# Kernel tuning notes

Measured on AMD Instinct MI355X. Metric: run time of the kernel, lower is better.

## Reference

```python
import jax, jax.numpy as jnp
import numpy as np
import math

B, S, D, H = 2, 2048, 1024, 16
DK = D // H
NUM_BUCKETS = 32
MAX_DISTANCE = 128


def _relative_position_bucket(relative_position, num_buckets=NUM_BUCKETS, max_distance=MAX_DISTANCE):
    # Bidirectional bucketing, faithful to the torch implementation.
    nb = num_buckets // 2
    n = -relative_position
    ret = (n < 0).astype(jnp.int32) * nb
    n = jnp.abs(n)
    max_exact = nb // 2
    is_small = n < max_exact
    # guard log(0); is_small branch covers n < max_exact anyway
    val_if_large = max_exact + (
        jnp.log(jnp.maximum(n, 1).astype(jnp.float32) / max_exact)
        / math.log(max_distance / max_exact)
        * (nb - max_exact)
    ).astype(jnp.int32)
    val_if_large = jnp.minimum(val_if_large, nb - 1)
    return ret + jnp.where(is_small, n, val_if_large)


def setup_inputs() -> dict:
    key = jax.random.key(0)
    ks = jax.random.split(key, 6)
    scale = 1.0 / math.sqrt(D)
    return {
        "hidden_states": jax.random.normal(ks[0], (B, S, D), dtype=jnp.float32),
        "Wq": jax.random.normal(ks[1], (D, D), dtype=jnp.float32) * scale,
        "Wk": jax.random.normal(ks[2], (D, D), dtype=jnp.float32) * scale,
        "Wv": jax.random.normal(ks[3], (D, D), dtype=jnp.float32) * scale,
        "Wo": jax.random.normal(ks[4], (D, D), dtype=jnp.float32) * scale,
        "rel_emb": jax.random.normal(ks[5], (NUM_BUCKETS, H), dtype=jnp.float32) * 0.1,
    }


def reference(hidden_states, Wq, Wk, Wv, Wo, rel_emb):
    b, s, d = hidden_states.shape
    # nn.Linear convention: y = x @ W.T
    q = jnp.einsum("bsd,ed->bse", hidden_states, Wq).reshape(b, s, H, DK).transpose(0, 2, 1, 3)
    k = jnp.einsum("bsd,ed->bse", hidden_states, Wk).reshape(b, s, H, DK).transpose(0, 2, 1, 3)
    v = jnp.einsum("bsd,ed->bse", hidden_states, Wv).reshape(b, s, H, DK).transpose(0, 2, 1, 3)
    scores = jnp.einsum("bhqd,bhkd->bhqk", q, k) / math.sqrt(DK)  # [B,H,S,S]
    # T5 relative position bias
    ctx = jnp.arange(s)[:, None]
    mem = jnp.arange(s)[None, :]
    rp_bucket = _relative_position_bucket(mem - ctx)          # [S,S]
    bias = rel_emb[rp_bucket]                                  # [S,S,H]
    bias = bias.transpose(2, 0, 1)[None]                       # [1,H,S,S]
    scores = scores + bias
    attn = jax.nn.softmax(scores, axis=-1)
    out = jnp.einsum("bhqk,bhkd->bhqd", attn, v)               # [B,H,S,DK]
    out = out.transpose(0, 2, 1, 3).reshape(b, s, d)
    return jnp.einsum("bsd,ed->bse", out, Wo)
```

## Files before the change

### kernel.cpp

```cpp
#include <hip/hip_runtime.h>
#include <hip/hip_bf16.h>
#include <cstdint>
#include <cstddef>

typedef __bf16 bf16;
typedef __attribute__((ext_vector_type(8))) __bf16 bf16x8;
typedef __attribute__((ext_vector_type(4))) __bf16 bf16x4;
typedef __attribute__((ext_vector_type(4))) float f32x4;
typedef __attribute__((ext_vector_type(4))) short s16x4;

#define B_ 2
#define S_ 2048
#define D_ 1024
#define H_ 16
#define DK_ 64
#define NROWS (B_*S_)
#define NBIAS 4095
#define LDQ 3072
#define LOG2E 1.44269504f

__device__ __forceinline__ void async16(void* lds, const void* g) {
  __builtin_amdgcn_global_load_lds(
      (const __attribute__((address_space(1))) void*)g,
      (__attribute__((address_space(3))) void*)lds, 16, 0, 0);
}

__device__ __forceinline__ f32x4 mfma16(bf16x8 a, bf16x8 b, f32x4 c) {
  return __builtin_amdgcn_mfma_f32_16x16x32_bf16(a, b, c, 0, 0, 0);
}

__device__ __forceinline__ s16x4 bc4(bf16x4 x) {
  union { bf16x4 b; s16x4 s; } u; u.b = x; return u.s;
}

__device__ __forceinline__ f32x4 mfma16k(bf16x4 a, bf16x4 b, f32x4 c) {
  return __builtin_amdgcn_mfma_f32_16x16x16bf16_1k(bc4(a), bc4(b), c, 0, 0, 0);
}

__device__ __forceinline__ float exp2_hw(float x) {
  return __builtin_amdgcn_exp2f(x);
}

__global__ void prep_kernel(const float* __restrict__ X,
                            const float* __restrict__ Wq, const float* __restrict__ Wk,
                            const float* __restrict__ Wv, const float* __restrict__ Wo,
                            const float* __restrict__ rel_emb,
                            bf16* __restrict__ Xb, bf16* __restrict__ oqkv,
                            bf16* __restrict__ oo, float* __restrict__ tab) {
  const int bid = blockIdx.x;
  const int tid = threadIdx.x;
  if (bid < 4096) {
    int i = bid * 256 + tid;
    float4 v = ((const float4*)X)[i];
    bf16x4 o;
    o[0] = (bf16)v.x; o[1] = (bf16)v.y; o[2] = (bf16)v.z; o[3] = (bf16)v.w;
    ((bf16x4*)Xb)[i] = o;
  } else if (bid < 8192) {
    int widx = bid - 4096;
    int y = widx >> 10;
    const float* src = (y == 0) ? Wq : (y == 1) ? Wk : (y == 2) ? Wv : Wo;
    bf16* dst = (y < 3) ? (oqkv + (size_t)y * D_ * D_) : oo;
    int i = (widx & 1023) * 256 + tid;
    float4 v = ((const float4*)src)[i];
    bf16x4 o;
    o[0] = (bf16)v.x; o[1] = (bf16)v.y; o[2] = (bf16)v.z; o[3] = (bf16)v.w;
    ((bf16x4*)dst)[i] = o;
  } else {
    int idx = (bid - 8192) * 256 + tid;
    if (idx >= H_ * NBIAS) return;
    int h = idx / NBIAS;
    int p = idx - h * NBIAS;
    int rel = p - 2047;
    int n = -rel;
    int ret = 0;
    if (n < 0) { ret = 16; n = -n; }
    int bucket;
    if (n < 8) {
      bucket = ret + n;
    } else {
      double v = log((double)n / 8.0) / log(16.0) * 8.0;
      int vi = 8 + (int)v;
      if (vi > 15) vi = 15;
      bucket = ret + vi;
    }
    tab[idx] = rel_emb[bucket * H_ + h] * LOG2E;
  }
}

template<int OUT_BF16, int MF, int VT_EP>
__global__ __launch_bounds__(256, 3)
void gemm_bt(const bf16* __restrict__ A, const bf16* __restrict__ Bw,
             void* __restrict__ C, bf16* __restrict__ VT, int vThr,
             int M, int N, int K, int colThr, float a0, float a1) {
  __shared__ bf16 smem[MF * 32 * 64 + 128 * 64];
  bf16* As = smem;
  bf16* Bs = smem + MF * 32 * 64;
  const int tid = threadIdx.x;
  const int lane = tid & 63;
  const int w = tid >> 6;
  const int wr = w >> 1, wc = w & 1;
  const int l15 = lane & 15, lhi = lane >> 4;
  const int m0 = blockIdx.y * (MF * 32), n0 = blockIdx.x * 128;
  const float alpha = (n0 < colThr) ? a0 : a1;

  f32x4 acc[MF][4] = {};

  const int urow = tid >> 3;
  const int uswz = (tid & 7) ^ (urow & 7);
  const bf16* ga = A  + (size_t)(m0 + urow) * K + uswz * 8;
  const bf16* gb = Bw + (size_t)(n0 + urow) * K + uswz * 8;

  for (int kt = 0; kt < K; kt += 64) {
#pragma unroll
    for (int rnd = 0; rnd < MF; ++rnd)
      async16(As + tid * 8 + rnd * 2048, ga + kt + (size_t)(rnd * 32) * K);
#pragma unroll
    for (int rnd = 0; rnd < 4; ++rnd)
      async16(Bs + tid * 8 + rnd * 2048, gb + kt + (size_t)(rnd * 32) * K);
    __syncthreads();

#pragma unroll
    for (int kc = 0; kc < 2; ++kc) {
      bf16x8 af[MF], bfr[4];
#pragma unroll
      for (int m = 0; m < MF; ++m) {
        int row = wr * (MF * 16) + m * 16 + l15;
        int off = (row * 64 + kc * 32 + lhi * 8) ^ ((row & 7) << 3);
        af[m] = *(const bf16x8*)&As[off];
      }
#pragma unroll
      for (int n = 0; n < 4; ++n) {
        int row = wc * 64 + n * 16 + l15;
        int off = (row * 64 + kc * 32 + lhi * 8) ^ ((row & 7) << 3);
        bfr[n] = *(const bf16x8*)&Bs[off];
      }
      __builtin_amdgcn_s_setprio(1);
#pragma unroll
      for (int m = 0; m < MF; ++m)
#pragma unroll
        for (int n = 0; n < 4; ++n)
          acc[m][n] = mfma16(af[m], bfr[n], acc[m][n]);
      __builtin_amdgcn_s_setprio(0);
    }
    __syncthreads();
  }

  if (VT_EP && n0 >= vThr) {
    bf16* T = smem;
#pragma unroll
    for (int m = 0; m < MF; ++m)
#pragma unroll
      for (int n = 0; n < 4; ++n)
#pragma unroll
        for (int r = 0; r < 4; ++r) {
          int rl = wr * (MF * 16) + m * 16 + lhi * 4 + r;
          int cl = wc * 64 + n * 16 + l15;
          T[cl * 128 + (rl ^ ((cl & 7) << 3))] = (bf16)(acc[m][n][r] * alpha);
        }
    __syncthreads();
    const int bb = m0 >> 11, s0l = m0 & 2047, d0 = n0 - vThr;
    const int dr = tid >> 1, sh = tid & 1;
    bf16* dst = VT + ((size_t)(bb * 1024 + d0 + dr)) * 2048 + s0l + sh * 64;
    const bf16* src = T + dr * 128;
#pragma unroll
    for (int i = 0; i < 8; ++i) {
      int sb = sh * 8 + i;
      *(bf16x8*)(dst + i * 8) = *(const bf16x8*)(src + ((sb ^ (dr & 7)) * 8));
    }
    return;
  }

#pragma unroll
  for (int m = 0; m < MF; ++m)
#pragma unroll
    for (int n = 0; n < 4; ++n)
#pragma unroll
      for (int r = 0; r < 4; ++r) {
        int row = m0 + wr * (MF * 16) + m * 16 + lhi * 4 + r;
        int col = n0 + wc * 64 + n * 16 + l15;
        float v = acc[m][n][r] * alpha;
        if (OUT_BF16) ((bf16*)C)[(size_t)row * N + col] = (bf16)v;
        else          ((float*)C)[(size_t)row * N + col] = v;
      }
}

__global__ __launch_bounds__(256, 2)
void attn_fwd(const bf16* __restrict__ QKV, const bf16* __restrict__ VTg_,
              const float* __restrict__ biasTab, const float* __restrict__ rel_emb,
              bf16* __restrict__ Og) {
  __shared__ bf16 Ks[2][64 * 64];
  __shared__ bf16 VTs[2][64 * 64];
  __shared__ float bias_s[512];
  const int tid = threadIdx.x;
  const int lane = tid & 63, w = tid >> 6;
  const int l15 = lane & 15, lhi = lane >> 4;
  const int wg = blockIdx.x;
  const int bh = wg & 31, qt = wg >> 5;
  const int b = bh >> 4, h = bh & 15;
  const int q0 = qt * 128;

  for (int i = tid; i < 511; i += 256)
    bias_s[i] = biasTab[h * NBIAS + 1792 + i];

  const float cL = rel_emb[15 * H_ + h] * LOG2E;
  const float cR = rel_emb[31 * H_ + h] * LOG2E;

  bf16x8 qa[2][2];
  {
    const bf16* Qbase = QKV + (size_t)(b * S_ + q0 + w * 32) * LDQ + h * DK_;
#pragma unroll
    for (int qf = 0; qf < 2; ++qf)
#pragma unroll
      for (int c = 0; c < 2; ++c)
        qa[qf][c] = *(const bf16x8*)(Qbase + (size_t)(qf * 16 + l15) * LDQ + c * 32 + lhi * 8);
  }

  int koff[8];
#pragma unroll
  for (int kf = 0; kf < 4; ++kf)
#pragma unroll
    for (int c = 0; c < 2; ++c) {
      int krow = kf * 16 + l15;
      koff[kf * 2 + c] = ((krow * 64 + c * 32 + lhi * 8) ^ ((krow & 7) << 3)) * 2;
    }
  int voff[16];
#pragma unroll
  for (int df = 0; df < 4; ++df)
#pragma unroll
    for (int kf = 0; kf < 4; ++kf)
      voff[df * 4 + kf] =
          (((df * 16 + l15) * 64 + kf * 16 + lhi * 4) * 2) ^ ((l15 & 7) << 4);

  float lpart[2] = {0.f, 0.f};
  f32x4 oacc[2][4] = {};

  const int urow = tid >> 3;
  const int uswz = (tid & 7) ^ (urow & 7);
  const bf16* gk = QKV  + (size_t)(b * S_) * LDQ + 1024 + h * DK_
                        + (size_t)urow * LDQ + uswz * 8;
  const bf16* gv = VTg_ + (size_t)(b * 1024 + h * DK_) * 2048
                        + (size_t)urow * 2048 + uswz * 8;

  async16(&Ks[0][tid * 8],         gk);
  async16(&Ks[0][tid * 8 + 2048],  gk + 32 * LDQ);
  async16(&VTs[0][tid * 8],        gv);
  async16(&VTs[0][tid * 8 + 2048], gv + 32 * 2048);
  gk += 64 * LDQ;
  gv += 64;
  __syncthreads();

#define TILE_BODY(CUR, KT, DO_PF)                                              \
  do {                                                                         \
    if (DO_PF) {                                                               \
      async16(&Ks[(CUR) ^ 1][tid * 8],         gk);                            \
      async16(&Ks[(CUR) ^ 1][tid * 8 + 2048],  gk + 32 * LDQ);                 \
      async16(&VTs[(CUR) ^ 1][tid * 8],        gv);                            \
      async16(&VTs[(CUR) ^ 1][tid * 8 + 2048], gv + 32 * 2048);                \
      gk += 64 * LDQ;                                                          \
      gv += 64;                                                                \
    }                                                                          \
    const int dk0 = (KT) - q0;                                                 \
    f32x4 st[2][4];                                                            \
    if (dk0 >= -128 && dk0 <= 192) {                                           \
      const int bb0 = dk0 + lhi * 4 - w * 32 - l15 + 255;                      \
      _Pragma("unroll")                                                        \
      for (int qf = 0; qf < 2; ++qf)                                           \
        _Pragma("unroll")                                                      \
        for (int kf = 0; kf < 4; ++kf)                                         \
          _Pragma("unroll")                                                    \
          for (int r = 0; r < 4; ++r)                                          \
            st[qf][kf][r] = bias_s[bb0 + (kf - qf) * 16 + r];                  \
    } else {                                                                   \
      const float cq = (dk0 > 0) ? cR : cL;                                    \
      _Pragma("unroll")                                                        \
      for (int qf = 0; qf < 2; ++qf)                                           \
        _Pragma("unroll")                                                      \
        for (int kf = 0; kf < 4; ++kf)                                         \
          _Pragma("unroll")                                                    \
          for (int r = 0; r < 4; ++r)                                          \
            st[qf][kf][r] = cq;                                                \
    }                                                                          \
    _Pragma("unroll")                                                          \
    for (int kf = 0; kf < 4; ++kf) {                                           \
      _Pragma("unroll")                                                        \
      for (int c = 0; c < 2; ++c) {                                            \
        bf16x8 kb = *(const bf16x8*)((const char*)&Ks[CUR][0] +                \
                                     koff[kf * 2 + c]);                        \
        st[0][kf] = mfma16(kb, qa[0][c], st[0][kf]);                           \
        st[1][kf] = mfma16(kb, qa[1][c], st[1][kf]);                           \
      }                                                                        \
    }                                                                          \
    bf16x4 pa[2][4];                                                           \
    _Pragma("unroll")                                                          \
    for (int qf = 0; qf < 2; ++qf) {                                           \
      float rs = 0.f;                                                          \
      _Pragma("unroll")                                                        \
      for (int kf = 0; kf < 4; ++kf)                                           \
        _Pragma("unroll")                                                      \
        for (int r = 0; r < 4; ++r) {                                          \
          float p = exp2_hw(st[qf][kf][r]);                                    \
          rs += p;                                                             \
          pa[qf][kf][r] = (bf16)p;                                             \
        }                                                                      \
      lpart[qf] += rs;                                                         \
    }                                                                          \
    _Pragma("unroll")                                                          \
    for (int df = 0; df < 4; ++df) {                                           \
      bf16x4 vb[4];                                                            \
      _Pragma("unroll")                                                        \
      for (int kf = 0; kf < 4; ++kf)                                           \
        vb[kf] = *(const bf16x4*)((const char*)&VTs[CUR][0] +                  \
                                  voff[df * 4 + kf]);                          \
      _Pragma("unroll")                                                        \
      for (int qf = 0; qf < 2; ++qf)                                           \
        _Pragma("unroll")                                                      \
        for (int kf = 0; kf < 4; ++kf)                                         \
          oacc[qf][df] = mfma16k(pa[qf][kf], vb[kf], oacc[qf][df]);            \
    }                                                                          \
    __syncthreads();                                                           \
  } while (0)

  for (int tt = 0; tt < 16; ++tt) {
    const int ktbase = tt * 128;
    TILE_BODY(0, ktbase, true);
    TILE_BODY(1, ktbase + 64, tt < 15);
  }
#undef TILE_BODY

#pragma unroll
  for (int qf = 0; qf < 2; ++qf) {
    float lr0 = lpart[qf];
    lr0 += __shfl_xor(lr0, 16);
    lr0 += __shfl_xor(lr0, 32);
#pragma unroll
    for (int r = 0; r < 4; ++r) {
      float lr = __shfl(lr0, lhi * 4 + r);
      float inv = 1.0f / lr;
#pragma unroll
      for (int df = 0; df < 4; ++df) {
        int row = b * S_ + q0 + w * 32 + qf * 16 + lhi * 4 + r;
        int col = h * DK_ + df * 16 + l15;
        Og[(size_t)row * D_ + col] = (bf16)(oacc[qf][df][r] * inv);
      }
    }
  }
}

extern "C" void kernel_launch(void* const* d_in, const int* in_sizes, int n_in,
                              void* d_out, int out_size, void* d_ws, size_t ws_size,
                              hipStream_t stream) {
  const float* X   = (const float*)d_in[0];
  const float* Wq  = (const float*)d_in[1];
  const float* Wk  = (const float*)d_in[2];
  const float* Wv  = (const float*)d_in[3];
  const float* Wo  = (const float*)d_in[4];
  const float* rel = (const float*)d_in[5];
  float* out = (float*)d_out;
  char* ws = (char*)d_ws;
  const size_t MB = 1u << 20;
  bf16* Xb    = (bf16*)(ws + 0 * MB);
  bf16* Wqkvb = (bf16*)(ws + 8 * MB);
  bf16* Wob   = (bf16*)(ws + 14 * MB);
  bf16* QKVb  = (bf16*)(ws + 16 * MB);
  bf16* VTb   = (bf16*)(ws + 40 * MB);
  float* biasTab = (float*)(ws + 48 * MB);

  prep_kernel<<<8448, 256, 0, stream>>>(X, Wq, Wk, Wv, Wo, rel,
                                        Xb, Wqkvb, Wob, biasTab);

  gemm_bt<1, 4, 1><<<dim3(24, 32), 256, 0, stream>>>(Xb, Wqkvb, QKVb,
      VTb, 2048,
      NROWS, 3 * D_, D_, 1024, 0.125f * LOG2E, 1.0f);

  attn_fwd<<<512, 256, 0, stream>>>(QKVb, VTb, biasTab, rel, Xb );

  gemm_bt<0, 2, 0><<<dim3(8, 64), 256, 0, stream>>>(Xb, Wob, out,
      nullptr, 1 << 30,
      NROWS, D_, D_, 0, 1.0f, 1.0f);
}
```

Measured before the change: 111.7 us.

## Split attention key range across two wave groups with LDS reduction

Attention blocks grow to 512 threads. Two groups of four waves each handle half of the key sequence for the same 128 query rows, with separate double-buffered K and V^T tiles in one shared-memory array. Because the softmax has no running max, the partial outputs and row sums can simply be added: the second group writes its accumulators to LDS and the first group adds them and normalizes. This halves the serial key loop per block and doubles the waves per CU to hide latency, at the cost of more LDS, a reduction step, and tighter register limits from the launch bounds.

```diff
diff --git a/kernel.cpp b/kernel.cpp
--- a/kernel.cpp
+++ b/kernel.cpp
@@ -184,22 +184,23 @@
       }
 }
 
-__global__ __launch_bounds__(256, 2)
+__global__ __launch_bounds__(512, 4)
 void attn_fwd(const bf16* __restrict__ QKV, const bf16* __restrict__ VTg_,
               const float* __restrict__ biasTab, const float* __restrict__ rel_emb,
               bf16* __restrict__ Og) {
-  __shared__ bf16 Ks[2][64 * 64];
-  __shared__ bf16 VTs[2][64 * 64];
+  __shared__ bf16 smemAll[8][64 * 64];
   __shared__ float bias_s[512];
   const int tid = threadIdx.x;
   const int lane = tid & 63, w = tid >> 6;
+  const int wl = w & 3, h2 = w >> 2;
   const int l15 = lane & 15, lhi = lane >> 4;
   const int wg = blockIdx.x;
   const int bh = wg & 31, qt = wg >> 5;
   const int b = bh >> 4, h = bh & 15;
   const int q0 = qt * 128;
-
-  for (int i = tid; i < 511; i += 256)
+  const int h1024 = h2 << 10;
+
+  for (int i = tid; i < 511; i += 512)
     bias_s[i] = biasTab[h * NBIAS + 1792 + i];
 
   const float cL = rel_emb[15 * H_ + h] * LOG2E;
@@ -207,7 +208,7 @@
 
   bf16x8 qa[2][2];
   {
-    const bf16* Qbase = QKV + (size_t)(b * S_ + q0 + w * 32) * LDQ + h * DK_;
+    const bf16* Qbase = QKV + (size_t)(b * S_ + q0 + wl * 32) * LDQ + h * DK_;
 #pragma unroll
     for (int qf = 0; qf < 2; ++qf)
 #pragma unroll
@@ -231,38 +232,41 @@
       voff[df * 4 + kf] =
           (((df * 16 + l15) * 64 + kf * 16 + lhi * 4) * 2) ^ ((l15 & 7) << 4);
 
+  const char* kbase = (const char*)&smemAll[h2 * 2][0];
+  const char* vbase = (const char*)&smemAll[4 + h2 * 2][0];
+
   float lpart[2] = {0.f, 0.f};
   f32x4 oacc[2][4] = {};
 
   const int urow = tid >> 3;
   const int uswz = (tid & 7) ^ (urow & 7);
-  const bf16* gk = QKV  + (size_t)(b * S_) * LDQ + 1024 + h * DK_
-                        + (size_t)urow * LDQ + uswz * 8;
-  const bf16* gv = VTg_ + (size_t)(b * 1024 + h * DK_) * 2048
-                        + (size_t)urow * 2048 + uswz * 8;
-
-  async16(&Ks[0][tid * 8],         gk);
-  async16(&Ks[0][tid * 8 + 2048],  gk + 32 * LDQ);
-  async16(&VTs[0][tid * 8],        gv);
-  async16(&VTs[0][tid * 8 + 2048], gv + 32 * 2048);
-  gk += 64 * LDQ;
-  gv += 64;
+  const bf16* gk0 = QKV  + (size_t)(b * S_) * LDQ + 1024 + h * DK_
+                         + (size_t)urow * LDQ + uswz * 8;
+  const bf16* gk1 = gk0 + (size_t)1024 * LDQ;
+  const bf16* gv0 = VTg_ + (size_t)(b * 1024 + h * DK_) * 2048
+                         + (size_t)urow * 2048 + uswz * 8;
+  const bf16* gv1 = gv0 + 1024;
+
+  async16(&smemAll[0][tid * 8], gk0);
+  async16(&smemAll[2][tid * 8], gk1);
+  async16(&smemAll[4][tid * 8], gv0);
+  async16(&smemAll[6][tid * 8], gv1);
+  gk0 += 64 * LDQ; gk1 += 64 * LDQ; gv0 += 64; gv1 += 64;
   __syncthreads();
 
 #define TILE_BODY(CUR, KT, DO_PF)                                              \
   do {                                                                         \
     if (DO_PF) {                                                               \
-      async16(&Ks[(CUR) ^ 1][tid * 8],         gk);                            \
-      async16(&Ks[(CUR) ^ 1][tid * 8 + 2048],  gk + 32 * LDQ);                 \
-      async16(&VTs[(CUR) ^ 1][tid * 8],        gv);                            \
-      async16(&VTs[(CUR) ^ 1][tid * 8 + 2048], gv + 32 * 2048);                \
-      gk += 64 * LDQ;                                                          \
-      gv += 64;                                                                \
+      async16(&smemAll[0 + ((CUR) ^ 1)][tid * 8], gk0);                        \
+      async16(&smemAll[2 + ((CUR) ^ 1)][tid * 8], gk1);                        \
+      async16(&smemAll[4 + ((CUR) ^ 1)][tid * 8], gv0);                        \
+      async16(&smemAll[6 + ((CUR) ^ 1)][tid * 8], gv1);                        \
+      gk0 += 64 * LDQ; gk1 += 64 * LDQ; gv0 += 64; gv1 += 64;                  \
     }                                                                          \
-    const int dk0 = (KT) - q0;                                                 \
+    const int dk0 = h1024 + (KT) - q0;                                         \
     f32x4 st[2][4];                                                            \
     if (dk0 >= -128 && dk0 <= 192) {                                           \
-      const int bb0 = dk0 + lhi * 4 - w * 32 - l15 + 255;                      \
+      const int bb0 = dk0 + lhi * 4 - wl * 32 - l15 + 255;                     \
       _Pragma("unroll")                                                        \
       for (int qf = 0; qf < 2; ++qf)                                           \
         _Pragma("unroll")                                                      \
@@ -284,8 +288,7 @@
     for (int kf = 0; kf < 4; ++kf) {                                           \
       _Pragma("unroll")                                                        \
       for (int c = 0; c < 2; ++c) {                                            \
-        bf16x8 kb = *(const bf16x8*)((const char*)&Ks[CUR][0] +                \
-                                     koff[kf * 2 + c]);                        \
+        bf16x8 kb = *(const bf16x8*)(kbase + (CUR) * 8192 + koff[kf * 2 + c]); \
         st[0][kf] = mfma16(kb, qa[0][c], st[0][kf]);                           \
         st[1][kf] = mfma16(kb, qa[1][c], st[1][kf]);                           \
       }                                                                        \
@@ -309,8 +312,7 @@
       bf16x4 vb[4];                                                            \
       _Pragma("unroll")                                                        \
       for (int kf = 0; kf < 4; ++kf)                                           \
-        vb[kf] = *(const bf16x4*)((const char*)&VTs[CUR][0] +                  \
-                                  voff[df * 4 + kf]);                          \
+        vb[kf] = *(const bf16x4*)(vbase + (CUR) * 8192 + voff[df * 4 + kf]);   \
       _Pragma("unroll")                                                        \
       for (int qf = 0; qf < 2; ++qf)                                           \
         _Pragma("unroll")                                                      \
@@ -320,27 +322,54 @@
     __syncthreads();                                                           \
   } while (0)
 
-  for (int tt = 0; tt < 16; ++tt) {
+  for (int tt = 0; tt < 8; ++tt) {
     const int ktbase = tt * 128;
     TILE_BODY(0, ktbase, true);
-    TILE_BODY(1, ktbase + 64, tt < 15);
+    TILE_BODY(1, ktbase + 64, tt < 7);
   }
 #undef TILE_BODY
 
-#pragma unroll
-  for (int qf = 0; qf < 2; ++qf) {
-    float lr0 = lpart[qf];
-    lr0 += __shfl_xor(lr0, 16);
-    lr0 += __shfl_xor(lr0, 32);
-#pragma unroll
-    for (int r = 0; r < 4; ++r) {
-      float lr = __shfl(lr0, lhi * 4 + r);
-      float inv = 1.0f / lr;
-#pragma unroll
-      for (int df = 0; df < 4; ++df) {
-        int row = b * S_ + q0 + w * 32 + qf * 16 + lhi * 4 + r;
-        int col = h * DK_ + df * 16 + l15;
-        Og[(size_t)row * D_ + col] = (bf16)(oacc[qf][df][r] * inv);
+  {
+    float* M = (float*)&smemAll[0][0];
+    const int slot = (wl * 64 + lane) * 36;
+    if (h2 == 1) {
+#pragma unroll
+      for (int qf = 0; qf < 2; ++qf)
+#pragma unroll
+        for (int df = 0; df < 4; ++df)
+          *(f32x4*)(M + slot + (qf * 4 + df) * 4) = oacc[qf][df];
+      M[slot + 32] = lpart[0];
+      M[slot + 33] = lpart[1];
+    }
+    __syncthreads();
+    if (h2 == 0) {
+#pragma unroll
+      for (int qf = 0; qf < 2; ++qf)
+#pragma unroll
+        for (int df = 0; df < 4; ++df) {
+          f32x4 o2 = *(const f32x4*)(M + slot + (qf * 4 + df) * 4);
+#pragma unroll
+          for (int r = 0; r < 4; ++r) oacc[qf][df][r] += o2[r];
+        }
+      lpart[0] += M[slot + 32];
+      lpart[1] += M[slot + 33];
+
+#pragma unroll
+      for (int qf = 0; qf < 2; ++qf) {
+        float lr0 = lpart[qf];
+        lr0 += __shfl_xor(lr0, 16);
+        lr0 += __shfl_xor(lr0, 32);
+#pragma unroll
+        for (int r = 0; r < 4; ++r) {
+          float lr = __shfl(lr0, lhi * 4 + r);
+          float inv = 1.0f / lr;
+#pragma unroll
+          for (int df = 0; df < 4; ++df) {
+            int row = b * S_ + q0 + wl * 32 + qf * 16 + lhi * 4 + r;
+            int col = h * DK_ + df * 16 + l15;
+            Og[(size_t)row * D_ + col] = (bf16)(oacc[qf][df][r] * inv);
+          }
+        }
       }
     }
   }
@@ -372,7 +401,7 @@
       VTb, 2048,
       NROWS, 3 * D_, D_, 1024, 0.125f * LOG2E, 1.0f);
 
-  attn_fwd<<<512, 256, 0, stream>>>(QKVb, VTb, biasTab, rel, Xb );
+  attn_fwd<<<512, 512, 0, stream>>>(QKVb, VTb, biasTab, rel, Xb );
 
   gemm_bt<0, 2, 0><<<dim3(8, 64), 256, 0, stream>>>(Xb, Wob, out,
       nullptr, 1 << 30,
```

Result: slower. 149.0 us (+33.4%).

## Triple-buffer K/V tiles with partial vmcnt waits in attention loop

Applied to the files above, without the earlier changes.

Moves the attention kernel's K and V^T LDS staging from double to triple buffering, keeping two tiles of async global-to-LDS loads in flight. The full __syncthreads is replaced by an explicit s_waitcnt vmcnt(4) plus s_barrier, so each step waits only for the oldest tile. The loop is restructured into rotations of three tiles with a drained tail. This raises LDS use per block, which may limit occupancy, and the manual waitcnt accounting must match the actual load count.

```diff
diff --git a/kernel.cpp b/kernel.cpp
--- a/kernel.cpp
+++ b/kernel.cpp
@@ -188,8 +188,8 @@
 void attn_fwd(const bf16* __restrict__ QKV, const bf16* __restrict__ VTg_,
               const float* __restrict__ biasTab, const float* __restrict__ rel_emb,
               bf16* __restrict__ Og) {
-  __shared__ bf16 Ks[2][64 * 64];
-  __shared__ bf16 VTs[2][64 * 64];
+  __shared__ bf16 Ks[3][64 * 64];
+  __shared__ bf16 VTs[3][64 * 64];
   __shared__ float bias_s[512];
   const int tid = threadIdx.x;
   const int lane = tid & 63, w = tid >> 6;
@@ -245,19 +245,23 @@
   async16(&Ks[0][tid * 8 + 2048],  gk + 32 * LDQ);
   async16(&VTs[0][tid * 8],        gv);
   async16(&VTs[0][tid * 8 + 2048], gv + 32 * 2048);
-  gk += 64 * LDQ;
-  gv += 64;
-  __syncthreads();
-
-#define TILE_BODY(CUR, KT, DO_PF)                                              \
+  gk += 64 * LDQ;  gv += 64;
+  async16(&Ks[1][tid * 8],         gk);
+  async16(&Ks[1][tid * 8 + 2048],  gk + 32 * LDQ);
+  async16(&VTs[1][tid * 8],        gv);
+  async16(&VTs[1][tid * 8 + 2048], gv + 32 * 2048);
+  gk += 64 * LDQ;  gv += 64;
+  asm volatile("s_waitcnt vmcnt(4) lgkmcnt(0)" ::: "memory");
+  __builtin_amdgcn_s_barrier();
+
+#define TILE_BODY(CUR, NXT, KT, DO_PF, WAITSTR)                                \
   do {                                                                         \
     if (DO_PF) {                                                               \
-      async16(&Ks[(CUR) ^ 1][tid * 8],         gk);                            \
-      async16(&Ks[(CUR) ^ 1][tid * 8 + 2048],  gk + 32 * LDQ);                 \
-      async16(&VTs[(CUR) ^ 1][tid * 8],        gv);                            \
-      async16(&VTs[(CUR) ^ 1][tid * 8 + 2048], gv + 32 * 2048);                \
-      gk += 64 * LDQ;                                                          \
-      gv += 64;                                                                \
+      async16(&Ks[NXT][tid * 8],         gk);                                  \
+      async16(&Ks[NXT][tid * 8 + 2048],  gk + 32 * LDQ);                       \
+      async16(&VTs[NXT][tid * 8],        gv);                                  \
+      async16(&VTs[NXT][tid * 8 + 2048], gv + 32 * 2048);                      \
+      gk += 64 * LDQ;  gv += 64;                                               \
     }                                                                          \
     const int dk0 = (KT) - q0;                                                 \
     f32x4 st[2][4];                                                            \
@@ -317,14 +321,18 @@
         for (int kf = 0; kf < 4; ++kf)                                         \
           oacc[qf][df] = mfma16k(pa[qf][kf], vb[kf], oacc[qf][df]);            \
     }                                                                          \
-    __syncthreads();                                                           \
+    asm volatile("s_waitcnt " WAITSTR ::: "memory");                           \
+    __builtin_amdgcn_s_barrier();                                              \
   } while (0)
 
-  for (int tt = 0; tt < 16; ++tt) {
-    const int ktbase = tt * 128;
-    TILE_BODY(0, ktbase, true);
-    TILE_BODY(1, ktbase + 64, tt < 15);
-  }
+  for (int rr = 0; rr < 10; ++rr) {
+    const int ktb = rr * 192;
+    TILE_BODY(0, 2, ktb,       true,  "vmcnt(4)");
+    TILE_BODY(1, 0, ktb + 64,  true,  "vmcnt(4)");
+    TILE_BODY(2, 1, ktb + 128, true,  "vmcnt(4)");
+  }
+  TILE_BODY(0, 0, 1920, false, "vmcnt(0)");
+  TILE_BODY(1, 0, 1984, false, "vmcnt(0)");
 #undef TILE_BODY
 
 #pragma unroll
```

Measured after the change: 109.6 us (median of 2 runs). No clear change (-1.8%).

## Split attention keys across two workgroups and merge partial outputs

Applied to the files above, without the earlier changes.

Each attention workgroup now processes half of the key sequence, doubling the grid to 1024 workgroups, and launch bounds are raised to 4 waves per SIMD. Unnormalized partial outputs are written to spare workspace regions along with per-row softmax denominators. A new merge kernel sums the two partials and normalizes them before the output projection. This targets low occupancy and CU underuse in attention, at the cost of an extra kernel, extra global traffic, and bf16 rounding of the partials.

```diff
diff --git a/kernel.cpp b/kernel.cpp
--- a/kernel.cpp
+++ b/kernel.cpp
@@ -184,10 +184,11 @@
       }
 }
 
-__global__ __launch_bounds__(256, 2)
+__global__ __launch_bounds__(256, 4)
 void attn_fwd(const bf16* __restrict__ QKV, const bf16* __restrict__ VTg_,
               const float* __restrict__ biasTab, const float* __restrict__ rel_emb,
-              bf16* __restrict__ Og) {
+              bf16* __restrict__ Op0, bf16* __restrict__ Op1,
+              float* __restrict__ Lws) {
   __shared__ bf16 Ks[2][64 * 64];
   __shared__ bf16 VTs[2][64 * 64];
   __shared__ float bias_s[512];
@@ -195,9 +196,12 @@
   const int lane = tid & 63, w = tid >> 6;
   const int l15 = lane & 15, lhi = lane >> 4;
   const int wg = blockIdx.x;
-  const int bh = wg & 31, qt = wg >> 5;
+  const int bh = wg & 31;
+  const int rest = wg >> 5;
+  const int qt = rest >> 1, h3 = rest & 1;
   const int b = bh >> 4, h = bh & 15;
   const int q0 = qt * 128;
+  const int kvbase = h3 << 10;
 
   for (int i = tid; i < 511; i += 256)
     bias_s[i] = biasTab[h * NBIAS + 1792 + i];
@@ -236,17 +240,16 @@
 
   const int urow = tid >> 3;
   const int uswz = (tid & 7) ^ (urow & 7);
-  const bf16* gk = QKV  + (size_t)(b * S_) * LDQ + 1024 + h * DK_
+  const bf16* gk = QKV  + (size_t)(b * S_ + kvbase) * LDQ + 1024 + h * DK_
                         + (size_t)urow * LDQ + uswz * 8;
-  const bf16* gv = VTg_ + (size_t)(b * 1024 + h * DK_) * 2048
+  const bf16* gv = VTg_ + (size_t)(b * 1024 + h * DK_) * 2048 + kvbase
                         + (size_t)urow * 2048 + uswz * 8;
 
   async16(&Ks[0][tid * 8],         gk);
   async16(&Ks[0][tid * 8 + 2048],  gk + 32 * LDQ);
   async16(&VTs[0][tid * 8],        gv);
   async16(&VTs[0][tid * 8 + 2048], gv + 32 * 2048);
-  gk += 64 * LDQ;
-  gv += 64;
+  gk += 64 * LDQ;  gv += 64;
   __syncthreads();
 
 #define TILE_BODY(CUR, KT, DO_PF)                                              \
@@ -256,10 +259,9 @@
       async16(&Ks[(CUR) ^ 1][tid * 8 + 2048],  gk + 32 * LDQ);                 \
       async16(&VTs[(CUR) ^ 1][tid * 8],        gv);                            \
       async16(&VTs[(CUR) ^ 1][tid * 8 + 2048], gv + 32 * 2048);                \
-      gk += 64 * LDQ;                                                          \
-      gv += 64;                                                                \
+      gk += 64 * LDQ;  gv += 64;                                               \
     }                                                                          \
-    const int dk0 = (KT) - q0;                                                 \
+    const int dk0 = kvbase + (KT) - q0;                                        \
     f32x4 st[2][4];                                                            \
     if (dk0 >= -128 && dk0 <= 192) {                                           \
       const int bb0 = dk0 + lhi * 4 - w * 32 - l15 + 255;                      \
@@ -320,13 +322,16 @@
     __syncthreads();                                                           \
   } while (0)
 
-  for (int tt = 0; tt < 16; ++tt) {
+  for (int tt = 0; tt < 8; ++tt) {
     const int ktbase = tt * 128;
     TILE_BODY(0, ktbase, true);
-    TILE_BODY(1, ktbase + 64, tt < 15);
+    TILE_BODY(1, ktbase + 64, tt < 7);
   }
 #undef TILE_BODY
 
+  bf16* Op = h3 ? Op1 : Op0;
+  const int ostride = h3 ? LDQ : D_;
+  const int obase = h3 ? 2048 : 0;
 #pragma unroll
   for (int qf = 0; qf < 2; ++qf) {
     float lr0 = lpart[qf];
@@ -335,15 +340,31 @@
 #pragma unroll
     for (int r = 0; r < 4; ++r) {
       float lr = __shfl(lr0, lhi * 4 + r);
-      float inv = 1.0f / lr;
-#pragma unroll
-      for (int df = 0; df < 4; ++df) {
-        int row = b * S_ + q0 + w * 32 + qf * 16 + lhi * 4 + r;
-        int col = h * DK_ + df * 16 + l15;
-        Og[(size_t)row * D_ + col] = (bf16)(oacc[qf][df][r] * inv);
-      }
+      int row = b * S_ + q0 + w * 32 + qf * 16 + lhi * 4 + r;
+      if (l15 == 0) Lws[(h3 * H_ + h) * NROWS + row] = lr;
+#pragma unroll
+      for (int df = 0; df < 4; ++df)
+        Op[(size_t)row * ostride + obase + h * DK_ + df * 16 + l15] =
+            (bf16)oacc[qf][df][r];
     }
   }
+}
+
+__global__ __launch_bounds__(256)
+void merge_kernel(const bf16* __restrict__ O0, const bf16* __restrict__ O1,
+                  const float* __restrict__ L, bf16* __restrict__ Out) {
+  int idx = blockIdx.x * 256 + threadIdx.x;
+  int row = idx >> 7;
+  int col = (idx & 127) * 8;
+  int h = col >> 6;
+  float inv = 1.0f / (L[h * NROWS + row] + L[(H_ + h) * NROWS + row]);
+  bf16x8 a = *(const bf16x8*)(O0 + (size_t)row * D_ + col);
+  bf16x8 c = *(const bf16x8*)(O1 + (size_t)row * LDQ + 2048 + col);
+  bf16x8 o;
+#pragma unroll
+  for (int j = 0; j < 8; ++j)
+    o[j] = (bf16)(((float)a[j] + (float)c[j]) * inv);
+  *(bf16x8*)(Out + (size_t)row * D_ + col) = o;
 }
 
 extern "C" void kernel_launch(void* const* d_in, const int* in_sizes, int n_in,
@@ -364,6 +385,7 @@
   bf16* QKVb  = (bf16*)(ws + 16 * MB);
   bf16* VTb   = (bf16*)(ws + 40 * MB);
   float* biasTab = (float*)(ws + 48 * MB);
+  float* Lws  = (float*)(ws + 49 * MB);
 
   prep_kernel<<<8448, 256, 0, stream>>>(X, Wq, Wk, Wv, Wo, rel,
                                         Xb, Wqkvb, Wob, biasTab);
@@ -372,9 +394,12 @@
       VTb, 2048,
       NROWS, 3 * D_, D_, 1024, 0.125f * LOG2E, 1.0f);
 
-  attn_fwd<<<512, 256, 0, stream>>>(QKVb, VTb, biasTab, rel, Xb );
-
-  gemm_bt<0, 2, 0><<<dim3(8, 64), 256, 0, stream>>>(Xb, Wob, out,
+  attn_fwd<<<1024, 256, 0, stream>>>(QKVb, VTb, biasTab, rel,
+                                     Xb, QKVb, Lws);
+
+  merge_kernel<<<2048, 256, 0, stream>>>(Xb, QKVb, Lws, VTb);
+
+  gemm_bt<0, 2, 0><<<dim3(8, 64), 256, 0, stream>>>(VTb, Wob, out,
       nullptr, 1 << 30,
       NROWS, D_, D_, 0, 1.0f, 1.0f);
 }
```

Measured after the change: 130.8 us. 1.17x slower.
